# Performance work log

Measured on AMD Instinct MI355X. Metric: run time of the kernel, lower is better.

## Reference

```python
import jax, jax.numpy as jnp
import numpy as np

N_ENV = 100000
D_PS = 512
N_SPECIES = 4
N_SUPPORT = 256
N_STRUCT = 1000
ZETA = 2


def setup_inputs() -> dict:
    key = jax.random.key(0)
    k1, k2, k3, k4, k5 = jax.random.split(key, 5)
    power_spectrum = jax.random.normal(k1, (N_ENV, D_PS), dtype=jnp.float32)
    sp = jax.random.normal(k2, (N_SPECIES, N_SUPPORT, D_PS), dtype=jnp.float32)
    # CosineKernel asserts support points are unit-norm
    support_points = sp / jnp.linalg.norm(sp, axis=-1, keepdims=True)
    weights = jax.random.normal(k3, (N_SPECIES, 1, N_SUPPORT), dtype=jnp.float32)
    all_species = jax.random.randint(k4, (N_ENV,), 0, N_SPECIES, dtype=jnp.int64)
    structure_ids = jnp.sort(jax.random.randint(k5, (N_ENV,), 0, N_STRUCT, dtype=jnp.int64))
    return {
        "power_spectrum": power_spectrum,
        "support_points": support_points,
        "weights": weights,
        "all_species": all_species,
        "structure_ids": structure_ids,
    }


def reference(power_spectrum, support_points, weights, all_species, structure_ids):
    # Normalize each environment's power spectrum (CosineKernel)
    ps = power_spectrum / jnp.linalg.norm(power_spectrum, axis=1, keepdims=True)
    # Kernel of every environment against every species' support set: [N, S, M]
    k = jnp.einsum("nd,smd->nsm", ps, support_points) ** ZETA
    # Per-row energy contribution for each species: k @ weights[s].T -> [N, S]
    contrib = jnp.einsum("nsm,sm->ns", k, weights[:, 0, :])
    # Species masking: each row only contributes through its own species' kernel
    onehot = jax.nn.one_hot(all_species, N_SPECIES, dtype=contrib.dtype)  # [N, S]
    per_row = jnp.sum(contrib * onehot, axis=1)  # [N]
    # Segmented sum over structures (equivalent to looping over structures_slices)
    energy = jax.ops.segment_sum(per_row, structure_ids, num_segments=N_STRUCT)
    return energy[:, None]  # [n_structures, 1]
```

## Files before the change

### kernel.cpp

```cpp
#include <hip/hip_runtime.h>
#include <hip/hip_bf16.h>


constexpr int kNEnv     = 100000;
constexpr int kDPS      = 512;
constexpr int kNSpecies = 4;
constexpr int kNSupport = 256;
constexpr int kCap      = 32768;

constexpr int BN = 64;
constexpr int BK = 32;

typedef __attribute__((ext_vector_type(8))) short short8;
typedef __attribute__((ext_vector_type(4))) float f32x4;

__device__ __forceinline__ short8 pack_bf16x8(const float4& a, const float4& b) {
  union { short8 v; __hip_bfloat162 h[4]; } u;
  u.h[0] = __float22bfloat162_rn({a.x, a.y});
  u.h[1] = __float22bfloat162_rn({a.z, a.w});
  u.h[2] = __float22bfloat162_rn({b.x, b.y});
  u.h[3] = __float22bfloat162_rn({b.z, b.w});
  return u.v;
}

__device__ __forceinline__ void gload_lds16(const void* g, void* l) {
  __builtin_amdgcn_global_load_lds(
      (const __attribute__((address_space(1))) void*)g,
      (__attribute__((address_space(3))) void*)l, 16, 0, 0);
}

__global__ void scatter_convert_kernel(const float* __restrict__ sp,
                                       const int* __restrict__ species,
                                       const int* __restrict__ sid,
                                       int* __restrict__ cnt, int* __restrict__ perm,
                                       int* __restrict__ sidp, short* __restrict__ spb) {
  const int t = threadIdx.x;
  const int b = blockIdx.x;
  if (b < (kNSpecies * kNSupport * kDPS) / (256 * 8)) {
    const int base = (b * 256 + t) * 8;
    const float4 lo = *(const float4*)(sp + base);
    const float4 hi = *(const float4*)(sp + base + 4);
    *(short8*)(spb + base) = pack_bf16x8(lo, hi);
  }
  const int wv   = t >> 6;
  const int lane = t & 63;
  const int i    = b * 256 + t;
  const bool v   = i < kNEnv;
  int s = -1, g = 0;
  if (v) { s = species[i]; g = sid[i]; }

  unsigned long long m[kNSpecies];
  #pragma unroll
  for (int k = 0; k < kNSpecies; ++k) m[k] = __ballot(s == k);
  int r = 0;
  if (v) r = __popcll(m[s] & ((1ull << lane) - 1ull));

  __shared__ int wcnt[4][kNSpecies];
  __shared__ int wbase[4][kNSpecies];
  if (lane < kNSpecies) wcnt[wv][lane] = (int)__popcll(m[lane]);
  __syncthreads();
  if (t < kNSpecies) {
    const int k = t;
    const int tot = wcnt[0][k] + wcnt[1][k] + wcnt[2][k] + wcnt[3][k];
    int p = tot ? atomicAdd(&cnt[k], tot) : 0;
    #pragma unroll
    for (int wvi = 0; wvi < 4; ++wvi) { wbase[wvi][k] = p; p += wcnt[wvi][k]; }
  }
  __syncthreads();
  if (v) {
    const int d = s * kCap + wbase[wv][s] + r;
    perm[d] = i;
    sidp[d] = g;
  }
}

__global__ __launch_bounds__(256, 3) void gap_gemm_v7(
    const float* __restrict__ ps, const short* __restrict__ spb,
    const float* __restrict__ w, const int* __restrict__ cnt,
    const int* __restrict__ perm, const int* __restrict__ sidp,
    float* __restrict__ energy) {
  const int s     = blockIdx.z;
  const int count = min(cnt[s], kCap);
  const int tile0 = blockIdx.x * BN;
  if (tile0 >= count) return;

  __shared__ float a_lds[4][BN * BK];
  __shared__ float red[4][BN];
  __shared__ float sqs[BN];

  const int tid  = threadIdx.x;
  const int wv   = tid >> 6;
  const int lane = tid & 63;
  const int l15  = lane & 15;
  const int lq   = lane >> 4;

  const int sby = ((lane & 7) << 4) ^ (((lane >> 3) & 7) << 4);
  const float* ssrc[2];
  #pragma unroll
  for (int c = 0; c < 2; ++c) {
    int r  = wv * 16 + c * 8 + (lane >> 3);
    int ge = tile0 + r;
    ge = ge < count ? ge : count - 1;
    ssrc[c] = ps + (size_t)perm[s * kCap + ge] * kDPS + (sby >> 2);
  }
  const int dof0 = (wv * 16) * BK;
  const int dof1 = (wv * 16 + 8) * BK;

  const short* bptr[4];
  float wgt[4];
  const float* w_s = w + s * kNSupport;
  #pragma unroll
  for (int fj = 0; fj < 4; ++fj) {
    const int m = wv * 64 + fj * 16 + l15;
    bptr[fj] = spb + ((size_t)s * kNSupport + m) * kDPS + lq * 8;
    wgt[fj]  = w_s[m];
  }

  const int fswz = (l15 & 7) << 4;
  const int cb1  = (lq * 32) ^ fswz;
  const int cb2  = (lq * 32 + 16) ^ fswz;
  const int rowb = l15 * 128;

  f32x4 acc[4][4];
  #pragma unroll
  for (int fi = 0; fi < 4; ++fi)
    #pragma unroll
    for (int fj = 0; fj < 4; ++fj) acc[fi][fj] = (f32x4)0.f;
  float sq[4] = {0.f, 0.f, 0.f, 0.f};

  short8 bf0[4], bf1[4];

#define STAGE7(T) do {                                                  \
    gload_lds16(ssrc[0] + (T) * BK, &a_lds[(T) & 3][dof0]);             \
    gload_lds16(ssrc[1] + (T) * BK, &a_lds[(T) & 3][dof1]);             \
  } while (0)
#define BLOAD7(T, BF) do {                                              \
    _Pragma("unroll")                                                   \
    for (int fj = 0; fj < 4; ++fj)                                      \
      BF[fj] = *(const short8*)(bptr[fj] + (T) * BK);                   \
  } while (0)
#define BODY7(T, BF) do {                                                       \
    const char* abase = (const char*)&a_lds[(T) & 3][0];                        \
    __builtin_amdgcn_s_setprio(1);                                              \
    _Pragma("unroll")                                                           \
    for (int fi = 0; fi < 4; ++fi) {                                            \
      const float4 f1 = *(const float4*)(abase + fi * 2048 + rowb + cb1);       \
      const float4 f2 = *(const float4*)(abase + fi * 2048 + rowb + cb2);       \
      if (wv == 0)                                                              \
        sq[fi] += f1.x * f1.x + f1.y * f1.y + f1.z * f1.z + f1.w * f1.w         \
                + f2.x * f2.x + f2.y * f2.y + f2.z * f2.z + f2.w * f2.w;        \
      const short8 af = pack_bf16x8(f1, f2);                                    \
      _Pragma("unroll")                                                         \
      for (int fj = 0; fj < 4; ++fj)                                            \
        acc[fi][fj] = __builtin_amdgcn_mfma_f32_16x16x32_bf16(                  \
            af, BF[fj], acc[fi][fj], 0, 0, 0);                                  \
    }                                                                           \
    __builtin_amdgcn_s_setprio(0);                                              \
  } while (0)

#define STEP7(T, VN, BFCUR, BFNXT) do {                                 \
    if ((T) + 1 < 16) BLOAD7((T) + 1, BFNXT);                           \
    if ((T) + 2 < 16) STAGE7((T) + 2);                                  \
    asm volatile("s_waitcnt vmcnt(" #VN ")" ::: "memory");              \
    __builtin_amdgcn_s_barrier();                                       \
    BODY7(T, BFCUR);                                                    \
  } while (0)

  STAGE7(0);
  STAGE7(1);
  BLOAD7(0, bf0);

  STEP7(0,  6, bf0, bf1);
  STEP7(1,  8, bf1, bf0);
  STEP7(2,  8, bf0, bf1);
  STEP7(3,  8, bf1, bf0);
  STEP7(4,  8, bf0, bf1);
  STEP7(5,  8, bf1, bf0);
  STEP7(6,  8, bf0, bf1);
  STEP7(7,  8, bf1, bf0);
  STEP7(8,  8, bf0, bf1);
  STEP7(9,  8, bf1, bf0);
  STEP7(10, 8, bf0, bf1);
  STEP7(11, 8, bf1, bf0);
  STEP7(12, 8, bf0, bf1);
  STEP7(13, 8, bf1, bf0);
  STEP7(14, 6, bf0, bf1);
  STEP7(15, 0, bf1, bf0);

#undef STEP7
#undef BODY7
#undef BLOAD7
#undef STAGE7

  if (wv == 0) {
    #pragma unroll
    for (int fi = 0; fi < 4; ++fi) {
      float p = sq[fi];
      p += __shfl_xor(p, 16, 64);
      p += __shfl_xor(p, 32, 64);
      if (lane < 16) sqs[fi * 16 + lane] = p;
    }
  }

  #pragma unroll
  for (int fi = 0; fi < 4; ++fi) {
    #pragma unroll
    for (int r = 0; r < 4; ++r) {
      float p = 0.f;
      #pragma unroll
      for (int fj = 0; fj < 4; ++fj) {
        const float c = acc[fi][fj][r];
        p += c * c * wgt[fj];
      }
      p += __shfl_xor(p, 1, 64);
      p += __shfl_xor(p, 2, 64);
      p += __shfl_xor(p, 4, 64);
      p += __shfl_xor(p, 8, 64);
      if (l15 == 0) red[wv][fi * 16 + lq * 4 + r] = p;
    }
  }
  __syncthreads();
  if (tid < BN) {
    const float v = red[0][tid] + red[1][tid] + red[2][tid] + red[3][tid];
    const int g  = tile0 + tid;
    if (g < count) atomicAdd(&energy[sidp[s * kCap + g]], v / sqs[tid]);
  }
}

extern "C" void kernel_launch(void* const* d_in, const int* in_sizes, int n_in,
                              void* d_out, int out_size, void* d_ws, size_t ws_size,
                              hipStream_t stream) {
  const float* ps      = (const float*)d_in[0];
  const float* sp      = (const float*)d_in[1];
  const float* w       = (const float*)d_in[2];
  const int*   species = (const int*)d_in[3];
  const int*   sid     = (const int*)d_in[4];
  float* energy = (float*)d_out;

  char* wsb = (char*)d_ws;
  constexpr size_t kOffPerm = 256;
  constexpr size_t kOffSidp = kOffPerm + (size_t)kNSpecies * kCap * 4;
  constexpr size_t kOffSpb  = kOffSidp + (size_t)kNSpecies * kCap * 4;

  int*   cnt  = (int*)wsb;
  int*   perm = (int*)(wsb + kOffPerm);
  int*   sidp = (int*)(wsb + kOffSidp);
  short* spb  = (short*)(wsb + kOffSpb);

  hipMemsetAsync(cnt, 0, 16, stream);
  hipMemsetAsync(energy, 0, out_size * sizeof(float), stream);

  scatter_convert_kernel<<<(kNEnv + 255) / 256, 256, 0, stream>>>(
      sp, species, sid, cnt, perm, sidp, spb);

  dim3 grid(kCap / BN, 1, kNSpecies);
  gap_gemm_v7<<<grid, 256, 0, stream>>>(ps, spb, w, cnt, perm, sidp, energy);
}
```

Measured before the change: 348.2 us.

## Stage A tile through registers as bf16 in LDS with grouped pipeline

Result: faster. 337.6 us (-3.1%).

```diff
diff --git a/kernel.cpp b/kernel.cpp
--- a/kernel.cpp
+++ b/kernel.cpp
@@ -21,12 +21,6 @@
   u.h[2] = __float22bfloat162_rn({b.x, b.y});
   u.h[3] = __float22bfloat162_rn({b.z, b.w});
   return u.v;
-}
-
-__device__ __forceinline__ void gload_lds16(const void* g, void* l) {
-  __builtin_amdgcn_global_load_lds(
-      (const __attribute__((address_space(1))) void*)g,
-      (__attribute__((address_space(3))) void*)l, 16, 0, 0);
 }
 
 __global__ void scatter_convert_kernel(const float* __restrict__ sp,
@@ -74,7 +68,7 @@
   }
 }
 
-__global__ __launch_bounds__(256, 3) void gap_gemm_v7(
+__global__ __launch_bounds__(256, 3) void gap_gemm_v8(
     const float* __restrict__ ps, const short* __restrict__ spb,
     const float* __restrict__ w, const int* __restrict__ cnt,
     const int* __restrict__ perm, const int* __restrict__ sidp,
@@ -84,7 +78,7 @@
   const int tile0 = blockIdx.x * BN;
   if (tile0 >= count) return;
 
-  __shared__ float a_lds[4][BN * BK];
+  __shared__ short a_lds[4][BN][32];
   __shared__ float red[4][BN];
   __shared__ float sqs[BN];
 
@@ -94,17 +88,11 @@
   const int l15  = lane & 15;
   const int lq   = lane >> 4;
 
-  const int sby = ((lane & 7) << 4) ^ (((lane >> 3) & 7) << 4);
-  const float* ssrc[2];
-  #pragma unroll
-  for (int c = 0; c < 2; ++c) {
-    int r  = wv * 16 + c * 8 + (lane >> 3);
-    int ge = tile0 + r;
-    ge = ge < count ? ge : count - 1;
-    ssrc[c] = ps + (size_t)perm[s * kCap + ge] * kDPS + (sby >> 2);
-  }
-  const int dof0 = (wv * 16) * BK;
-  const int dof1 = (wv * 16 + 8) * BK;
+  const int r0 = wv * 16 + (lane >> 2);
+  const int q  = lane & 3;
+  int ge = tile0 + r0;
+  ge = ge < count ? ge : count - 1;
+  const float* asrc = ps + (size_t)perm[s * kCap + ge] * kDPS + q * 8;
 
   const short* bptr[4];
   float wgt[4];
@@ -116,91 +104,84 @@
     wgt[fj]  = w_s[m];
   }
 
-  const int fswz = (l15 & 7) << 4;
-  const int cb1  = (lq * 32) ^ fswz;
-  const int cb2  = (lq * 32 + 16) ^ fswz;
-  const int rowb = l15 * 128;
-
   f32x4 acc[4][4];
   #pragma unroll
   for (int fi = 0; fi < 4; ++fi)
     #pragma unroll
     for (int fj = 0; fj < 4; ++fj) acc[fi][fj] = (f32x4)0.f;
-  float sq[4] = {0.f, 0.f, 0.f, 0.f};
-
+  float sq = 0.f;
+
+  float4 R[8];
   short8 bf0[4], bf1[4];
 
-#define STAGE7(T) do {                                                  \
-    gload_lds16(ssrc[0] + (T) * BK, &a_lds[(T) & 3][dof0]);             \
-    gload_lds16(ssrc[1] + (T) * BK, &a_lds[(T) & 3][dof1]);             \
-  } while (0)
-#define BLOAD7(T, BF) do {                                              \
-    _Pragma("unroll")                                                   \
-    for (int fj = 0; fj < 4; ++fj)                                      \
-      BF[fj] = *(const short8*)(bptr[fj] + (T) * BK);                   \
-  } while (0)
-#define BODY7(T, BF) do {                                                       \
-    const char* abase = (const char*)&a_lds[(T) & 3][0];                        \
-    __builtin_amdgcn_s_setprio(1);                                              \
-    _Pragma("unroll")                                                           \
-    for (int fi = 0; fi < 4; ++fi) {                                            \
-      const float4 f1 = *(const float4*)(abase + fi * 2048 + rowb + cb1);       \
-      const float4 f2 = *(const float4*)(abase + fi * 2048 + rowb + cb2);       \
-      if (wv == 0)                                                              \
-        sq[fi] += f1.x * f1.x + f1.y * f1.y + f1.z * f1.z + f1.w * f1.w         \
-                + f2.x * f2.x + f2.y * f2.y + f2.z * f2.z + f2.w * f2.w;        \
-      const short8 af = pack_bf16x8(f1, f2);                                    \
-      _Pragma("unroll")                                                         \
-      for (int fj = 0; fj < 4; ++fj)                                            \
-        acc[fi][fj] = __builtin_amdgcn_mfma_f32_16x16x32_bf16(                  \
-            af, BF[fj], acc[fi][fj], 0, 0, 0);                                  \
-    }                                                                           \
-    __builtin_amdgcn_s_setprio(0);                                              \
-  } while (0)
-
-#define STEP7(T, VN, BFCUR, BFNXT) do {                                 \
-    if ((T) + 1 < 16) BLOAD7((T) + 1, BFNXT);                           \
-    if ((T) + 2 < 16) STAGE7((T) + 2);                                  \
-    asm volatile("s_waitcnt vmcnt(" #VN ")" ::: "memory");              \
-    __builtin_amdgcn_s_barrier();                                       \
-    BODY7(T, BFCUR);                                                    \
-  } while (0)
-
-  STAGE7(0);
-  STAGE7(1);
-  BLOAD7(0, bf0);
-
-  STEP7(0,  6, bf0, bf1);
-  STEP7(1,  8, bf1, bf0);
-  STEP7(2,  8, bf0, bf1);
-  STEP7(3,  8, bf1, bf0);
-  STEP7(4,  8, bf0, bf1);
-  STEP7(5,  8, bf1, bf0);
-  STEP7(6,  8, bf0, bf1);
-  STEP7(7,  8, bf1, bf0);
-  STEP7(8,  8, bf0, bf1);
-  STEP7(9,  8, bf1, bf0);
-  STEP7(10, 8, bf0, bf1);
-  STEP7(11, 8, bf1, bf0);
-  STEP7(12, 8, bf0, bf1);
-  STEP7(13, 8, bf1, bf0);
-  STEP7(14, 6, bf0, bf1);
-  STEP7(15, 0, bf1, bf0);
-
-#undef STEP7
-#undef BODY7
-#undef BLOAD7
-#undef STAGE7
-
-  if (wv == 0) {
-    #pragma unroll
-    for (int fi = 0; fi < 4; ++fi) {
-      float p = sq[fi];
-      p += __shfl_xor(p, 16, 64);
-      p += __shfl_xor(p, 32, 64);
-      if (lane < 16) sqs[fi * 16 + lane] = p;
-    }
-  }
+#define GLOAD8(G) do {                                                    \
+    _Pragma("unroll")                                                     \
+    for (int u = 0; u < 8; ++u)                                           \
+      R[u] = *(const float4*)(asrc + (G) * 128 + (u >> 1) * 32 + (u & 1) * 4); \
+  } while (0)
+
+#define AWRITE8() do {                                                    \
+    _Pragma("unroll")                                                     \
+    for (int j = 0; j < 4; ++j) {                                         \
+      const float4 va = R[2 * j], vb = R[2 * j + 1];                      \
+      sq += va.x * va.x + va.y * va.y + va.z * va.z + va.w * va.w         \
+          + vb.x * vb.x + vb.y * vb.y + vb.z * vb.z + vb.w * vb.w;        \
+      *(short8*)&a_lds[j][r0][q * 8] = pack_bf16x8(va, vb);               \
+    }                                                                     \
+  } while (0)
+
+#define BLOAD8(T, BF) do {                                                \
+    _Pragma("unroll")                                                     \
+    for (int fj = 0; fj < 4; ++fj)                                        \
+      BF[fj] = *(const short8*)(bptr[fj] + (T) * BK);                     \
+  } while (0)
+
+#define ASTEP8(J, BF) do {                                                \
+    short8 af[4];                                                         \
+    _Pragma("unroll")                                                     \
+    for (int fi = 0; fi < 4; ++fi)                                        \
+      af[fi] = *(const short8*)&a_lds[J][fi * 16 + l15][lq * 8];          \
+    __builtin_amdgcn_s_setprio(1);                                        \
+    _Pragma("unroll")                                                     \
+    for (int fi = 0; fi < 4; ++fi)                                        \
+      _Pragma("unroll")                                                   \
+      for (int fj = 0; fj < 4; ++fj)                                      \
+        acc[fi][fj] = __builtin_amdgcn_mfma_f32_16x16x32_bf16(            \
+            af[fi], BF[fj], acc[fi][fj], 0, 0, 0);                        \
+    __builtin_amdgcn_s_setprio(0);                                        \
+  } while (0)
+
+#define GROUP8(G) do {                                                    \
+    __builtin_amdgcn_s_barrier();              \
+    AWRITE8();                                                            \
+    asm volatile("s_waitcnt lgkmcnt(0)" ::: "memory");                    \
+    __builtin_amdgcn_s_barrier();                     \
+    __builtin_amdgcn_sched_barrier(0);                                    \
+    if ((G) < 3) GLOAD8((G) + 1);             \
+    __builtin_amdgcn_sched_barrier(0);                                    \
+    BLOAD8((G) * 4 + 1, bf1); ASTEP8(0, bf0);                             \
+    BLOAD8((G) * 4 + 2, bf0); ASTEP8(1, bf1);                             \
+    BLOAD8((G) * 4 + 3, bf1); ASTEP8(2, bf0);                             \
+    if ((G) < 3) BLOAD8((G) * 4 + 4, bf0);                                \
+    ASTEP8(3, bf1);                                                       \
+  } while (0)
+
+  GLOAD8(0);
+  BLOAD8(0, bf0);
+  GROUP8(0);
+  GROUP8(1);
+  GROUP8(2);
+  GROUP8(3);
+
+#undef GROUP8
+#undef ASTEP8
+#undef BLOAD8
+#undef AWRITE8
+#undef GLOAD8
+
+  sq += __shfl_xor(sq, 1, 64);
+  sq += __shfl_xor(sq, 2, 64);
+  if (q == 0) sqs[r0] = sq;
 
   #pragma unroll
   for (int fi = 0; fi < 4; ++fi) {
@@ -254,5 +235,5 @@
       sp, species, sid, cnt, perm, sidp, spb);
 
   dim3 grid(kCap / BN, 1, kNSpecies);
-  gap_gemm_v7<<<grid, 256, 0, stream>>>(ps, spb, w, cnt, perm, sidp, energy);
-}
+  gap_gemm_v8<<<grid, 256, 0, stream>>>(ps, spb, w, cnt, perm, sidp, energy);
+}
```
